# Performance work log

Measured on AMD Instinct MI355X. Metric: run time of the kernel, lower is better.

## Reference

```python
import jax, jax.numpy as jnp
import numpy as np

B, N, E = 4, 8192, 131072
R, NUM_CLASSES, H, OUT = 16, 100, 128, 32


def _rgcn_layer(h, W, src, dst, rel, mask_edge):
    # h: [B,N,in], W: [R,in,out], src/dst/rel: [B,E] int, mask_edge: [B,E]
    # Per-edge msg = h[src] @ W[rel] * norm(=1); computed as per-relation
    # projection of all nodes followed by a (src, rel) gather.
    proj = jnp.einsum('bni,rio->bnro', h, W)          # [B,N,R,out]
    bidx = jnp.arange(B)[:, None]                      # [B,1]
    msg = proj[bidx, src, rel] * mask_edge[..., None]  # [B,E,out]
    # scatter-sum messages onto destination nodes (fn.sum in DGL)
    seg = (jnp.arange(B)[:, None] * N + dst).reshape(-1)
    out = jax.ops.segment_sum(msg.reshape(B * E, -1), seg, num_segments=B * N)
    return out.reshape(B, N, -1)


def setup_inputs() -> dict:
    key = jax.random.key(0)
    ks = jax.random.split(key, 10)
    class_objects = jax.random.randint(ks[0], (B, N), 0, NUM_CLASSES)
    states_objects = jax.random.normal(ks[1], (B, N, 8), dtype=jnp.float32)
    edge_tuples = jax.random.randint(ks[2], (B, E, 2), 0, N)
    edge_classes = jax.random.randint(ks[3], (B, E), 0, R)
    mask_object = jnp.ones((B, N), dtype=jnp.float32)
    mask_edge = jnp.ones((B, E), dtype=jnp.float32)
    embed = jax.random.normal(ks[4], (NUM_CLASSES, H), dtype=jnp.float32) * 0.05
    W1 = jax.random.normal(ks[5], (R, H, H), dtype=jnp.float32) * 0.05
    W2 = jax.random.normal(ks[6], (R, H, H), dtype=jnp.float32) * 0.05
    W3 = jax.random.normal(ks[7], (R, H, OUT), dtype=jnp.float32) * 0.05
    return {'class_objects': class_objects, 'states_objects': states_objects,
            'edge_tuples': edge_tuples, 'edge_classes': edge_classes,
            'mask_object': mask_object, 'mask_edge': mask_edge,
            'embed': embed, 'W1': W1, 'W2': W2, 'W3': W3}


def reference(class_objects, states_objects, edge_tuples, edge_classes,
              mask_object, mask_edge, embed, W1, W2, W3):
    src = edge_tuples[..., 0]
    dst = edge_tuples[..., 1]
    rel = edge_classes
    h = embed[class_objects]                                  # [B,N,H]
    h = jax.nn.relu(_rgcn_layer(h, W1, src, dst, rel, mask_edge))
    h = jax.nn.relu(_rgcn_layer(h, W2, src, dst, rel, mask_edge))
    h = jax.nn.softmax(_rgcn_layer(h, W3, src, dst, rel, mask_edge), axis=-1)
    # original pads each env's node features with zeros up to max_nodes
    return h * mask_object[..., None]                         # [B,N,OUT]
```

## Files before the change

### kernel.cpp

```cpp
#include <hip/hip_runtime.h>

typedef __attribute__((ext_vector_type(4))) float f32x4;
typedef __attribute__((ext_vector_type(8))) short short8;

#define B_ 4
#define N_ 8192
#define E_ 131072
#define R_ 16
#define H_ 128
#define OUT_ 32
#define NKEYS (B_*N_*R_)
#define NEDGE (B_*E_)

__device__ __forceinline__ unsigned short f2bf(float f){
  unsigned int u = __float_as_uint(f);
  u = (u + 0x7fffu + ((u>>16)&1u)) >> 16;
  return (unsigned short)u;
}
__device__ __forceinline__ float bfh(unsigned u, int hi){
  return __uint_as_float(hi ? (u & 0xffff0000u) : (u << 16));
}
__device__ __forceinline__ unsigned cvtpk(float lo, float hi){
  unsigned r;
  asm("v_cvt_pk_bf16_f32 %0, %1, %2" : "=v"(r) : "v"(lo), "v"(hi));
  return r;
}
__device__ __forceinline__ void glds16(const void* g, void* l){
  __builtin_amdgcn_global_load_lds((const __attribute__((address_space(1))) unsigned int*)g,
                                   (__attribute__((address_space(3))) unsigned int*)l,
                                   16, 0, 0);
}


__global__ void hist_k(const int* __restrict__ et, const int* __restrict__ ec,
                       int* __restrict__ cnt){
  int e = blockIdx.x*256 + threadIdx.x;
  int b = e >> 17;
  int dst = et[2*e+1];
  int r  = ec[e];
  atomicAdd(&cnt[(((b<<13)+dst)<<4) + r], 1);
}

__global__ void scanA_k(const int* __restrict__ cnt,
                        int* __restrict__ offp, int* __restrict__ cidxp,
                        int* __restrict__ bsumV, int* __restrict__ bsumF){
  __shared__ int ldsV[256], ldsF[256];
  int t = threadIdx.x;
  int base = blockIdx.x*1024 + t*4;
  int4 v = *(const int4*)(cnt + base);
  int4 f; f.x = v.x!=0; f.y = v.y!=0; f.z = v.z!=0; f.w = v.w!=0;
  ldsV[t] = v.x+v.y+v.z+v.w;
  ldsF[t] = f.x+f.y+f.z+f.w;
  __syncthreads();
  for (int off=1; off<256; off<<=1){
    int xv = (t>=off) ? ldsV[t-off] : 0;
    int xf = (t>=off) ? ldsF[t-off] : 0;
    __syncthreads();
    ldsV[t] += xv; ldsF[t] += xf;
    __syncthreads();
  }
  if (t==255){ bsumV[blockIdx.x] = ldsV[255]; bsumF[blockIdx.x] = ldsF[255]; }
  int pv = (t==0) ? 0 : ldsV[t-1];
  int pf = (t==0) ? 0 : ldsF[t-1];
  int4 ov; ov.x = pv; ov.y = ov.x+v.x; ov.z = ov.y+v.y; ov.w = ov.z+v.z;
  int4 of; of.x = pf; of.y = of.x+f.x; of.z = of.y+f.y; of.w = of.z+f.z;
  *(int4*)(offp  + base) = ov;
  *(int4*)(cidxp + base) = of;
}

__global__ void scanB_k(int* __restrict__ bsumV, int* __restrict__ bsumF){
  int* bs = blockIdx.x ? bsumF : bsumV;
  __shared__ int lds[256];
  int t = threadIdx.x;
  int2 v = *(const int2*)(bs + t*2);
  lds[t] = v.x+v.y;
  __syncthreads();
  for (int off=1; off<256; off<<=1){
    int x = (t>=off) ? lds[t-off] : 0;
    __syncthreads();
    lds[t] += x;
    __syncthreads();
  }
  int pre = (t==0) ? 0 : lds[t-1];
  int2 o; o.x = pre; o.y = pre + v.x;
  *(int2*)(bs + t*2) = o;
}

__global__ void scanC_k(const int* __restrict__ offp, const int* __restrict__ cidxp,
                        const int* __restrict__ bsumV, const int* __restrict__ bsumF,
                        const int* __restrict__ cnt,
                        int* __restrict__ off,
                        int* __restrict__ cmapA, int* __restrict__ cmapB,
                        uint4* __restrict__ kdesc, int aggcRow){
  int t = threadIdx.x;
  int base = blockIdx.x*1024 + t*4;
  int addV = bsumV[blockIdx.x];
  int addF = bsumF[blockIdx.x] + 1;
  int4 o  = *(const int4*)(offp + base);
  o.x+=addV; o.y+=addV; o.z+=addV; o.w+=addV;
  *(int4*)(off + base) = o;
  int4 cx = *(const int4*)(cidxp + base);
  int4 cv = *(const int4*)(cnt + base);
  int4 cm;
  cm.x = cv.x ? cx.x+addF : 0;
  cm.y = cv.y ? cx.y+addF : 0;
  cm.z = cv.z ? cx.z+addF : 0;
  cm.w = cv.w ? cx.w+addF : 0;
  int4 vr;
  vr.x = aggcRow + cm.x; vr.y = aggcRow + cm.y;
  vr.z = aggcRow + cm.z; vr.w = aggcRow + cm.w;
  *(int4*)(cmapA + base) = vr;
  *(int4*)(cmapB + base) = vr;
  *(int2*)&kdesc[base+0].x = make_int2(o.x, (cv.x<<20)|cm.x);
  *(int2*)&kdesc[base+1].x = make_int2(o.y, (cv.y<<20)|cm.y);
  *(int2*)&kdesc[base+2].x = make_int2(o.z, (cv.z<<20)|cm.z);
  *(int2*)&kdesc[base+3].x = make_int2(o.w, (cv.w<<20)|cm.w);
}

__global__ void fill_k(const int* __restrict__ et, const int* __restrict__ ec,
                       const float* __restrict__ me, int* __restrict__ off,
                       uint2* __restrict__ erec, uint4* __restrict__ kdesc,
                       int* __restrict__ cmapA, int* __restrict__ cmapB,
                       int hARow, int hBRow){
  int e = blockIdx.x*256 + threadIdx.x;
  int b = e >> 17;
  int src = et[2*e];
  int dst = et[2*e+1];
  int r  = ec[e];
  int key = (((b<<13)+dst)<<4) + r;
  unsigned mbits = __float_as_uint(me[e]);
  int pos = atomicAdd(&off[key], 1);
  erec[pos] = make_uint2((unsigned)src, mbits);
  uint2 kxy = *(const uint2*)&kdesc[key].x;
  if (pos == (int)kxy.x) {
    *(uint2*)&kdesc[key].z = make_uint2((unsigned)src, mbits);
    if ((kxy.y >> 20) == 1u && mbits == 0x3f800000u) {
      int noderow = (b<<13) + src;
      cmapA[key] = hARow + noderow;
      cmapB[key] = hBRow + noderow;
    }
  }
}


__global__ void prep_k(const int* __restrict__ cls, const float* __restrict__ emb,
                       const float* __restrict__ W1, const float* __restrict__ W2,
                       const float* __restrict__ W3,
                       unsigned short* __restrict__ h,
                       unsigned short* __restrict__ W1t,
                       unsigned short* __restrict__ W2t,
                       unsigned short* __restrict__ W3t,
                       unsigned short* __restrict__ aggc){
  int t = blockIdx.x*256 + threadIdx.x;
  if (blockIdx.x == 0 && threadIdx.x < 16) {
    *(uint4*)((char*)aggc + threadIdx.x*16) = make_uint4(0,0,0,0);
  }
  if (t < B_*N_*32) {
    int node = t>>5, c = t&31;
    int cl = cls[node];
    float4 v = *(const float4*)(emb + cl*H_ + c*4);
    uint2 o;
    o.x = f2bf(v.x) | ((unsigned int)f2bf(v.y)<<16);
    o.y = f2bf(v.z) | ((unsigned int)f2bf(v.w)<<16);
    *(uint2*)(h + node*H_ + c*4) = o;
  } else {
    int u = t - B_*N_*32;
    if (u < R_*H_*H_) {
      int k = u & 127, n = (u>>7) & 127, r = u >> 14;
      W1t[u] = f2bf(W1[(r*H_ + k)*H_ + n]);
    } else if (u < 2*R_*H_*H_) {
      int u2 = u - R_*H_*H_;
      int k = u2 & 127, n = (u2>>7) & 127, r = u2 >> 14;
      W2t[u2] = f2bf(W2[(r*H_ + k)*H_ + n]);
    } else {
      int u2 = u - 2*R_*H_*H_;
      if (u2 < R_*OUT_*H_) {
        int k = u2 & 127, n = (u2>>7) & 31, r = u2 >> 12;
        W3t[u2] = f2bf(W3[(r*H_ + k)*OUT_ + n]);
      }
    }
  }
}


__global__ __launch_bounds__(256) void agg_k(
    const unsigned short* __restrict__ h_in,
    const uint4* __restrict__ kdesc,
    const uint2* __restrict__ erec,
    unsigned short* __restrict__ aggc){
  const int orig = blockIdx.x;
  const int x    = orig & 7;
  const int b    = x >> 1;
  const int lb   = ((x & 1) << 10) + (orig >> 3);
  const int key  = (b << 17) + (lb << 6) + (threadIdx.x >> 2);
  const int q    = threadIdx.x & 3;
  uint4 kd = kdesc[key];
  int cnt = (int)(kd.y >> 20);
  if (cnt == 0) return;
  if (cnt == 1 && kd.w == 0x3f800000u) return;
  int cm = (int)(kd.y & 0xFFFFFu);
  const unsigned short* hb = h_in + ((size_t)b << 20);

  float fa[32];
  #pragma unroll
  for (int i=0;i<32;++i) fa[i] = 0.f;

#define UNP8(FP, V, M) do { \
  (FP)[0]+=M*bfh((V).x,0); (FP)[1]+=M*bfh((V).x,1); \
  (FP)[2]+=M*bfh((V).y,0); (FP)[3]+=M*bfh((V).y,1); \
  (FP)[4]+=M*bfh((V).z,0); (FP)[5]+=M*bfh((V).z,1); \
  (FP)[6]+=M*bfh((V).w,0); (FP)[7]+=M*bfh((V).w,1); \
} while(0)
#define MAC32(SRC, MB) do { \
  float m_ = __uint_as_float(MB); \
  const uint4* hp_ = (const uint4*)(hb + (((unsigned)(SRC))<<7) + (q<<5)); \
  uint4 v0_ = hp_[0], v1_ = hp_[1], v2_ = hp_[2], v3_ = hp_[3]; \
  UNP8(fa+0,  v0_, m_); UNP8(fa+8,  v1_, m_); \
  UNP8(fa+16, v2_, m_); UNP8(fa+24, v3_, m_); \
} while(0)

  int s = (int)kd.x;
  uint2 rc;
  if (cnt > 1) rc = erec[s+1];
  MAC32(kd.z, kd.w);
  for (int e = 1; e < cnt; ++e) {
    uint2 cur = rc;
    if (e+1 < cnt) rc = erec[s+e+1];
    MAC32(cur.x, cur.y);
  }
#undef MAC32
#undef UNP8

  unsigned short* ap = aggc + ((size_t)cm << 7) + (q<<5);
  #pragma unroll
  for (int c = 0; c < 4; ++c) {
    uint4 pk;
    pk.x = cvtpk(fa[c*8+0], fa[c*8+1]);
    pk.y = cvtpk(fa[c*8+2], fa[c*8+3]);
    pk.z = cvtpk(fa[c*8+4], fa[c*8+5]);
    pk.w = cvtpk(fa[c*8+6], fa[c*8+7]);
    *(uint4*)(ap + c*8) = pk;
  }
}


template<int NOUT>
__global__ __launch_bounds__((NOUT==128) ? 1024 : 512, 4) void gemm_k(
    const unsigned short* __restrict__ base,
    const int* __restrict__ cmap,
    const unsigned short* __restrict__ Wt,
    const float* __restrict__ mobj,
    unsigned short* __restrict__ h_out,
    float* __restrict__ out)
{
  constexpr int MT  = (NOUT==128) ? 128 : 64;
  constexpr int MI  = (NOUT==128) ? 2 : 1;
  constexpr int NIw = (NOUT==128) ? 2 : 1;
  __shared__ __align__(16) unsigned short A_s[3][MT*64];
  __shared__ __align__(16) unsigned short B_s[3][NOUT*64];
  __shared__ int cmap_s[MT*16];
  __shared__ float comb[(NOUT==32) ? 64*33 : 1];

  const int tid  = threadIdx.x;
  const int lane = tid & 63;
  const int w    = tid >> 6;
  const int c16  = lane & 15;
  const int g    = lane >> 4;
  const int m0   = blockIdx.x * MT;
  const int mbase = (NOUT==128) ? ((w>>2)<<5) : ((w>>1)<<4);
  const int nbase = (NOUT==128) ? ((w&3)<<5) : ((w&1)<<4);

  *(int2*)&cmap_s[tid<<1] = *(const int2*)(cmap + m0*16 + (tid<<1));
  __syncthreads();

#define STAGE(KC, BUF) do { \
  const int kc_ = (KC); \
  { \
    int m_ = tid>>3, u_ = tid&7; \
    int cm_ = cmap_s[(m_<<4) + (kc_>>1)]; \
    glds16((const char*)base + ((size_t)cm_<<8) + ((kc_&1)<<7) + ((u_ ^ (m_&7))<<4), \
           &A_s[BUF][tid<<3]); \
  } \
  if constexpr (NOUT==128) { \
    int n_ = tid>>3, u_ = tid&7; \
    glds16((const char*)Wt + ((size_t)((kc_>>1)*128 + n_)<<8) + ((kc_&1)<<7) + ((u_ ^ (n_&7))<<4), \
           &B_s[BUF][tid<<3]); \
  } else { \
    if (w < 4) { \
      int uid_ = (w<<6) + lane; \
      int n_ = uid_>>3, u_ = uid_&7; \
      glds16((const char*)Wt + ((size_t)((kc_>>1)*32 + n_)<<8) + ((kc_&1)<<7) + ((u_ ^ (n_&7))<<4), \
             &B_s[BUF][uid_<<3]); } \
  } \
} while(0)

#define WAIT_MAIN do { \
  if constexpr (NOUT==128) { asm volatile("s_waitcnt vmcnt(4)" ::: "memory"); } \
  else { if (w < 4) asm volatile("s_waitcnt vmcnt(4)" ::: "memory"); \
         else       asm volatile("s_waitcnt vmcnt(2)" ::: "memory"); } \
} while(0)
#define WAIT_T1 do { \
  if constexpr (NOUT==128) { asm volatile("s_waitcnt vmcnt(2)" ::: "memory"); } \
  else { if (w < 4) asm volatile("s_waitcnt vmcnt(2)" ::: "memory"); \
         else       asm volatile("s_waitcnt vmcnt(1)" ::: "memory"); } \
} while(0)

  f32x4 acc[MI][NIw];
  #pragma unroll
  for (int mi=0; mi<MI; ++mi)
    #pragma unroll
    for (int ni=0; ni<NIw; ++ni)
      acc[mi][ni] = f32x4{0.f,0.f,0.f,0.f};

#define COMPUTE(BUF) do { \
  _Pragma("unroll") \
  for (int kk=0; kk<2; ++kk) { \
    short8 af[MI], bfr[NIw]; \
    _Pragma("unroll") \
    for (int mi=0; mi<MI; ++mi) { \
      int m_ = mbase + mi*16 + c16; \
      af[mi] = *(const short8*)((const char*)&A_s[BUF][0] + m_*128 \
               + (((kk<<6) + (g<<4)) ^ ((m_&7)<<4))); } \
    _Pragma("unroll") \
    for (int ni=0; ni<NIw; ++ni) { \
      int n_ = nbase + ni*16 + c16; \
      bfr[ni] = *(const short8*)((const char*)&B_s[BUF][0] + n_*128 \
               + (((kk<<6) + (g<<4)) ^ ((n_&7)<<4))); } \
    _Pragma("unroll") \
    for (int mi=0; mi<MI; ++mi) \
      _Pragma("unroll") \
      for (int ni=0; ni<NIw; ++ni) \
        acc[mi][ni] = __builtin_amdgcn_mfma_f32_16x16x32_bf16(af[mi], bfr[ni], acc[mi][ni], 0,0,0); \
  } \
} while(0)

  STAGE(0, 0);
  STAGE(1, 1);
  for (int kc = 0; kc < 30; ++kc) {
    STAGE(kc+2, (kc+2)%3);
    WAIT_MAIN;
    __builtin_amdgcn_s_barrier();
    COMPUTE(kc%3);
    asm volatile("s_waitcnt lgkmcnt(0)" ::: "memory");
    __builtin_amdgcn_s_barrier();
  }
  WAIT_T1;
  __builtin_amdgcn_s_barrier();
  COMPUTE(0);
  asm volatile("s_waitcnt lgkmcnt(0)" ::: "memory");
  __builtin_amdgcn_s_barrier();
  asm volatile("s_waitcnt vmcnt(0)" ::: "memory");
  __builtin_amdgcn_s_barrier();
  COMPUTE(1);

  if constexpr (NOUT == 128) {
    #pragma unroll
    for (int mi=0; mi<MI; ++mi)
      #pragma unroll
      for (int ni=0; ni<NIw; ++ni)
        #pragma unroll
        for (int j=0; j<4; ++j) {
          int row = mbase + mi*16 + (g<<2) + j;
          int col = nbase + ni*16 + c16;
          h_out[((size_t)(m0+row)<<7) + col] = f2bf(fmaxf(acc[mi][ni][j], 0.f));
        }
  } else {
    #pragma unroll
    for (int j=0; j<4; ++j)
      comb[(mbase + (g<<2) + j)*33 + nbase + c16] = acc[0][0][j];
    __syncthreads();
    if (tid < 64) {
      const int row = tid;
      float v[32];
      #pragma unroll
      for (int c=0; c<32; ++c) v[c] = comb[row*33 + c];
      float mx = v[0];
      #pragma unroll
      for (int c=1; c<32; ++c) mx = fmaxf(mx, v[c]);
      float sm = 0.f;
      #pragma unroll
      for (int c=0; c<32; ++c){ v[c] = __expf(v[c]-mx); sm += v[c]; }
      float sc = mobj[m0+row] / sm;
      float4* op = (float4*)(out + ((size_t)(m0+row)<<5));
      #pragma unroll
      for (int c=0; c<8; ++c)
        op[c] = make_float4(v[4*c]*sc, v[4*c+1]*sc, v[4*c+2]*sc, v[4*c+3]*sc);
    }
  }
#undef STAGE
#undef WAIT_MAIN
#undef WAIT_T1
#undef COMPUTE
}

extern "C" void kernel_launch(void* const* d_in, const int* in_sizes, int n_in,
                              void* d_out, int out_size, void* d_ws, size_t ws_size,
                              hipStream_t stream){
  const int*   cls   = (const int*)  d_in[0];
  const int*   et    = (const int*)  d_in[2];
  const int*   ec    = (const int*)  d_in[3];
  const float* mobj  = (const float*)d_in[4];
  const float* medge = (const float*)d_in[5];
  const float* emb   = (const float*)d_in[6];
  const float* W1    = (const float*)d_in[7];
  const float* W2    = (const float*)d_in[8];
  const float* W3    = (const float*)d_in[9];
  float* out = (float*)d_out;

  char* ws = (char*)d_ws;
  size_t o = 0;
  auto alloc = [&](size_t bytes)->char*{
    char* p = ws + o;
    o += (bytes + 255) & ~(size_t)255;
    return p;
  };
  unsigned short* hA    = (unsigned short*)alloc((size_t)B_*N_*H_*2);
  unsigned short* hB    = (unsigned short*)alloc((size_t)B_*N_*H_*2);
  unsigned short* W1t   = (unsigned short*)alloc((size_t)R_*H_*H_*2);
  unsigned short* W2t   = (unsigned short*)alloc((size_t)R_*H_*H_*2);
  unsigned short* W3t   = (unsigned short*)alloc((size_t)R_*OUT_*H_*2);
  int*            cnt   = (int*)alloc((size_t)NKEYS*4);
  int*            off   = (int*)alloc((size_t)NKEYS*4);
  int*            offp  = (int*)alloc((size_t)NKEYS*4);
  int*            cidxp = (int*)alloc((size_t)NKEYS*4);
  int*            cmapA = (int*)alloc((size_t)NKEYS*4);
  int*            cmapB = (int*)alloc((size_t)NKEYS*4);
  int*            bsumV = (int*)alloc(512*4);
  int*            bsumF = (int*)alloc(512*4);
  uint4*          kdesc = (uint4*)alloc((size_t)NKEYS*16);
  uint2*          erec  = (uint2*)alloc((size_t)NEDGE*8);
  unsigned short* aggc  = (unsigned short*)alloc(((size_t)NKEYS+1)*H_*2);
  (void)ws_size; (void)in_sizes; (void)n_in; (void)out_size;

  const int hARow   = (int)(((char*)hA   - ws) >> 8);
  const int hBRow   = (int)(((char*)hB   - ws) >> 8);
  const int aggcRow = (int)(((char*)aggc - ws) >> 8);
  const unsigned short* vbase = (const unsigned short*)ws;

  hipMemsetAsync(cnt, 0, (size_t)NKEYS*4, stream);
  hipLaunchKernelGGL(hist_k,  dim3(NEDGE/256), dim3(256), 0, stream, et, ec, cnt);
  hipLaunchKernelGGL(scanA_k, dim3(512), dim3(256), 0, stream, cnt, offp, cidxp, bsumV, bsumF);
  hipLaunchKernelGGL(scanB_k, dim3(2),   dim3(256), 0, stream, bsumV, bsumF);
  hipLaunchKernelGGL(scanC_k, dim3(512), dim3(256), 0, stream, offp, cidxp, bsumV, bsumF,
                     cnt, off, cmapA, cmapB, kdesc, aggcRow);
  hipLaunchKernelGGL(fill_k,  dim3(NEDGE/256), dim3(256), 0, stream, et, ec, medge, off,
                     erec, kdesc, cmapA, cmapB, hARow, hBRow);

  hipLaunchKernelGGL(prep_k, dim3((B_*N_*32 + 2*R_*H_*H_ + R_*OUT_*H_)/256), dim3(256), 0, stream,
                     cls, emb, W1, W2, W3, hA, W1t, W2t, W3t, aggc);

  const int aggGrid = (NKEYS*4)/256;
  const int g128    = (B_*N_)/128;
  const int g32     = (B_*N_)/64;

  hipLaunchKernelGGL(agg_k, dim3(aggGrid), dim3(256), 0, stream, hA, kdesc, erec, aggc);
  hipLaunchKernelGGL((gemm_k<128>), dim3(g128), dim3(1024), 0, stream,
                     vbase, cmapA, W1t, (const float*)nullptr, hB, (float*)nullptr);
  hipLaunchKernelGGL(agg_k, dim3(aggGrid), dim3(256), 0, stream, hB, kdesc, erec, aggc);
  hipLaunchKernelGGL((gemm_k<128>), dim3(g128), dim3(1024), 0, stream,
                     vbase, cmapB, W2t, (const float*)nullptr, hA, (float*)nullptr);
  hipLaunchKernelGGL(agg_k, dim3(aggGrid), dim3(256), 0, stream, hA, kdesc, erec, aggc);
  hipLaunchKernelGGL((gemm_k<32>), dim3(g32), dim3(512), 0, stream,
                     vbase, cmapA, W3t, mobj, (unsigned short*)nullptr, out);
}
```

Before: 237.8 us.

## Replace counting-sort CSR build with atomicExch linked lists per key

```diff
diff --git a/kernel.cpp b/kernel.cpp
--- a/kernel.cpp
+++ b/kernel.cpp
@@ -11,6 +11,7 @@
 #define OUT_ 32
 #define NKEYS (B_*N_*R_)
 #define NEDGE (B_*E_)
+#define NEXT_MASK 0x7FFFFu
 
 __device__ __forceinline__ unsigned short f2bf(float f){
   unsigned int u = __float_as_uint(f);
@@ -32,114 +33,40 @@
 }
 
 
-__global__ void hist_k(const int* __restrict__ et, const int* __restrict__ ec,
-                       int* __restrict__ cnt){
+__global__ void link_k(const int* __restrict__ et, const int* __restrict__ ec,
+                       int* __restrict__ head, unsigned* __restrict__ link){
   int e = blockIdx.x*256 + threadIdx.x;
   int b = e >> 17;
-  int dst = et[2*e+1];
+  int2 sd = *(const int2*)(et + 2*e);
   int r  = ec[e];
-  atomicAdd(&cnt[(((b<<13)+dst)<<4) + r], 1);
-}
-
-__global__ void scanA_k(const int* __restrict__ cnt,
-                        int* __restrict__ offp, int* __restrict__ cidxp,
-                        int* __restrict__ bsumV, int* __restrict__ bsumF){
-  __shared__ int ldsV[256], ldsF[256];
-  int t = threadIdx.x;
-  int base = blockIdx.x*1024 + t*4;
-  int4 v = *(const int4*)(cnt + base);
-  int4 f; f.x = v.x!=0; f.y = v.y!=0; f.z = v.z!=0; f.w = v.w!=0;
-  ldsV[t] = v.x+v.y+v.z+v.w;
-  ldsF[t] = f.x+f.y+f.z+f.w;
-  __syncthreads();
-  for (int off=1; off<256; off<<=1){
-    int xv = (t>=off) ? ldsV[t-off] : 0;
-    int xf = (t>=off) ? ldsF[t-off] : 0;
-    __syncthreads();
-    ldsV[t] += xv; ldsF[t] += xf;
-    __syncthreads();
-  }
-  if (t==255){ bsumV[blockIdx.x] = ldsV[255]; bsumF[blockIdx.x] = ldsF[255]; }
-  int pv = (t==0) ? 0 : ldsV[t-1];
-  int pf = (t==0) ? 0 : ldsF[t-1];
-  int4 ov; ov.x = pv; ov.y = ov.x+v.x; ov.z = ov.y+v.y; ov.w = ov.z+v.z;
-  int4 of; of.x = pf; of.y = of.x+f.x; of.z = of.y+f.y; of.w = of.z+f.z;
-  *(int4*)(offp  + base) = ov;
-  *(int4*)(cidxp + base) = of;
-}
-
-__global__ void scanB_k(int* __restrict__ bsumV, int* __restrict__ bsumF){
-  int* bs = blockIdx.x ? bsumF : bsumV;
-  __shared__ int lds[256];
-  int t = threadIdx.x;
-  int2 v = *(const int2*)(bs + t*2);
-  lds[t] = v.x+v.y;
-  __syncthreads();
-  for (int off=1; off<256; off<<=1){
-    int x = (t>=off) ? lds[t-off] : 0;
-    __syncthreads();
-    lds[t] += x;
-    __syncthreads();
-  }
-  int pre = (t==0) ? 0 : lds[t-1];
-  int2 o; o.x = pre; o.y = pre + v.x;
-  *(int2*)(bs + t*2) = o;
-}
-
-__global__ void scanC_k(const int* __restrict__ offp, const int* __restrict__ cidxp,
-                        const int* __restrict__ bsumV, const int* __restrict__ bsumF,
-                        const int* __restrict__ cnt,
-                        int* __restrict__ off,
-                        int* __restrict__ cmapA, int* __restrict__ cmapB,
-                        uint4* __restrict__ kdesc, int aggcRow){
-  int t = threadIdx.x;
-  int base = blockIdx.x*1024 + t*4;
-  int addV = bsumV[blockIdx.x];
-  int addF = bsumF[blockIdx.x] + 1;
-  int4 o  = *(const int4*)(offp + base);
-  o.x+=addV; o.y+=addV; o.z+=addV; o.w+=addV;
-  *(int4*)(off + base) = o;
-  int4 cx = *(const int4*)(cidxp + base);
-  int4 cv = *(const int4*)(cnt + base);
-  int4 cm;
-  cm.x = cv.x ? cx.x+addF : 0;
-  cm.y = cv.y ? cx.y+addF : 0;
-  cm.z = cv.z ? cx.z+addF : 0;
-  cm.w = cv.w ? cx.w+addF : 0;
-  int4 vr;
-  vr.x = aggcRow + cm.x; vr.y = aggcRow + cm.y;
-  vr.z = aggcRow + cm.z; vr.w = aggcRow + cm.w;
-  *(int4*)(cmapA + base) = vr;
-  *(int4*)(cmapB + base) = vr;
-  *(int2*)&kdesc[base+0].x = make_int2(o.x, (cv.x<<20)|cm.x);
-  *(int2*)&kdesc[base+1].x = make_int2(o.y, (cv.y<<20)|cm.y);
-  *(int2*)&kdesc[base+2].x = make_int2(o.z, (cv.z<<20)|cm.z);
-  *(int2*)&kdesc[base+3].x = make_int2(o.w, (cv.w<<20)|cm.w);
-}
-
-__global__ void fill_k(const int* __restrict__ et, const int* __restrict__ ec,
-                       const float* __restrict__ me, int* __restrict__ off,
-                       uint2* __restrict__ erec, uint4* __restrict__ kdesc,
+  int key = (((b<<13)+sd.y)<<4) + r;
+  int old = atomicExch(&head[key], e);
+  unsigned nxt = (old < 0) ? (unsigned)e : (unsigned)old;
+  link[e] = (((unsigned)sd.x) << 19) | nxt;
+}
+
+
+__global__ void cmap_k(const int* __restrict__ head, const unsigned* __restrict__ link,
+                       const float* __restrict__ me,
                        int* __restrict__ cmapA, int* __restrict__ cmapB,
-                       int hARow, int hBRow){
-  int e = blockIdx.x*256 + threadIdx.x;
-  int b = e >> 17;
-  int src = et[2*e];
-  int dst = et[2*e+1];
-  int r  = ec[e];
-  int key = (((b<<13)+dst)<<4) + r;
-  unsigned mbits = __float_as_uint(me[e]);
-  int pos = atomicAdd(&off[key], 1);
-  erec[pos] = make_uint2((unsigned)src, mbits);
-  uint2 kxy = *(const uint2*)&kdesc[key].x;
-  if (pos == (int)kxy.x) {
-    *(uint2*)&kdesc[key].z = make_uint2((unsigned)src, mbits);
-    if ((kxy.y >> 20) == 1u && mbits == 0x3f800000u) {
-      int noderow = (b<<13) + src;
-      cmapA[key] = hARow + noderow;
-      cmapB[key] = hBRow + noderow;
+                       int hARow, int hBRow, int aggcRow){
+  int key = blockIdx.x*256 + threadIdx.x;
+  int hd = head[key];
+  int vA = aggcRow, vB = aggcRow;
+  if (hd >= 0) {
+    unsigned lk = link[hd];
+    int nxt = (int)(lk & NEXT_MASK);
+    if (nxt == hd && me[hd] == 1.0f) {
+      int noderow = ((key >> 17) << 13) + (int)(lk >> 19);
+      vA = hARow + noderow;
+      vB = hBRow + noderow;
+    } else {
+      vA = aggcRow + 1 + key;
+      vB = vA;
     }
   }
+  cmapA[key] = vA;
+  cmapB[key] = vB;
 }
 
 
@@ -185,8 +112,9 @@
 
 __global__ __launch_bounds__(256) void agg_k(
     const unsigned short* __restrict__ h_in,
-    const uint4* __restrict__ kdesc,
-    const uint2* __restrict__ erec,
+    const int* __restrict__ head,
+    const unsigned* __restrict__ link,
+    const float* __restrict__ me,
     unsigned short* __restrict__ aggc){
   const int orig = blockIdx.x;
   const int x    = orig & 7;
@@ -194,11 +122,12 @@
   const int lb   = ((x & 1) << 10) + (orig >> 3);
   const int key  = (b << 17) + (lb << 6) + (threadIdx.x >> 2);
   const int q    = threadIdx.x & 3;
-  uint4 kd = kdesc[key];
-  int cnt = (int)(kd.y >> 20);
-  if (cnt == 0) return;
-  if (cnt == 1 && kd.w == 0x3f800000u) return;
-  int cm = (int)(kd.y & 0xFFFFFu);
+  int hd = head[key];
+  if (hd < 0) return;
+  unsigned lk = link[hd];
+  int nxt = (int)(lk & NEXT_MASK);
+  float m0 = me[hd];
+  if (nxt == hd && m0 == 1.0f) return;
   const unsigned short* hb = h_in + ((size_t)b << 20);
 
   float fa[32];
@@ -211,27 +140,29 @@
   (FP)[4]+=M*bfh((V).z,0); (FP)[5]+=M*bfh((V).z,1); \
   (FP)[6]+=M*bfh((V).w,0); (FP)[7]+=M*bfh((V).w,1); \
 } while(0)
-#define MAC32(SRC, MB) do { \
-  float m_ = __uint_as_float(MB); \
+#define MAC32(SRC, M) do { \
   const uint4* hp_ = (const uint4*)(hb + (((unsigned)(SRC))<<7) + (q<<5)); \
   uint4 v0_ = hp_[0], v1_ = hp_[1], v2_ = hp_[2], v3_ = hp_[3]; \
-  UNP8(fa+0,  v0_, m_); UNP8(fa+8,  v1_, m_); \
-  UNP8(fa+16, v2_, m_); UNP8(fa+24, v3_, m_); \
-} while(0)
-
-  int s = (int)kd.x;
-  uint2 rc;
-  if (cnt > 1) rc = erec[s+1];
-  MAC32(kd.z, kd.w);
-  for (int e = 1; e < cnt; ++e) {
-    uint2 cur = rc;
-    if (e+1 < cnt) rc = erec[s+e+1];
-    MAC32(cur.x, cur.y);
+  UNP8(fa+0,  v0_, M); UNP8(fa+8,  v1_, M); \
+  UNP8(fa+16, v2_, M); UNP8(fa+24, v3_, M); \
+} while(0)
+
+  int cur = hd;
+  unsigned clk = lk;
+  float cm = m0;
+  for (;;) {
+    int src = (int)(clk >> 19);
+    MAC32(src, cm);
+    int nx = (int)(clk & NEXT_MASK);
+    if (nx == cur) break;
+    cur = nx;
+    clk = link[cur];
+    cm  = me[cur];
   }
 #undef MAC32
 #undef UNP8
 
-  unsigned short* ap = aggc + ((size_t)cm << 7) + (q<<5);
+  unsigned short* ap = aggc + (((size_t)(1 + key)) << 7) + (q<<5);
   #pragma unroll
   for (int c = 0; c < 4; ++c) {
     uint4 pk;
@@ -419,16 +350,10 @@
   unsigned short* W1t   = (unsigned short*)alloc((size_t)R_*H_*H_*2);
   unsigned short* W2t   = (unsigned short*)alloc((size_t)R_*H_*H_*2);
   unsigned short* W3t   = (unsigned short*)alloc((size_t)R_*OUT_*H_*2);
-  int*            cnt   = (int*)alloc((size_t)NKEYS*4);
-  int*            off   = (int*)alloc((size_t)NKEYS*4);
-  int*            offp  = (int*)alloc((size_t)NKEYS*4);
-  int*            cidxp = (int*)alloc((size_t)NKEYS*4);
+  int*            head  = (int*)alloc((size_t)NKEYS*4);
+  unsigned*       link  = (unsigned*)alloc((size_t)NEDGE*4);
   int*            cmapA = (int*)alloc((size_t)NKEYS*4);
   int*            cmapB = (int*)alloc((size_t)NKEYS*4);
-  int*            bsumV = (int*)alloc(512*4);
-  int*            bsumF = (int*)alloc(512*4);
-  uint4*          kdesc = (uint4*)alloc((size_t)NKEYS*16);
-  uint2*          erec  = (uint2*)alloc((size_t)NEDGE*8);
   unsigned short* aggc  = (unsigned short*)alloc(((size_t)NKEYS+1)*H_*2);
   (void)ws_size; (void)in_sizes; (void)n_in; (void)out_size;
 
@@ -437,14 +362,10 @@
   const int aggcRow = (int)(((char*)aggc - ws) >> 8);
   const unsigned short* vbase = (const unsigned short*)ws;
 
-  hipMemsetAsync(cnt, 0, (size_t)NKEYS*4, stream);
-  hipLaunchKernelGGL(hist_k,  dim3(NEDGE/256), dim3(256), 0, stream, et, ec, cnt);
-  hipLaunchKernelGGL(scanA_k, dim3(512), dim3(256), 0, stream, cnt, offp, cidxp, bsumV, bsumF);
-  hipLaunchKernelGGL(scanB_k, dim3(2),   dim3(256), 0, stream, bsumV, bsumF);
-  hipLaunchKernelGGL(scanC_k, dim3(512), dim3(256), 0, stream, offp, cidxp, bsumV, bsumF,
-                     cnt, off, cmapA, cmapB, kdesc, aggcRow);
-  hipLaunchKernelGGL(fill_k,  dim3(NEDGE/256), dim3(256), 0, stream, et, ec, medge, off,
-                     erec, kdesc, cmapA, cmapB, hARow, hBRow);
+  hipMemsetAsync(head, 0xFF, (size_t)NKEYS*4, stream);
+  hipLaunchKernelGGL(link_k, dim3(NEDGE/256), dim3(256), 0, stream, et, ec, head, link);
+  hipLaunchKernelGGL(cmap_k, dim3(NKEYS/256), dim3(256), 0, stream, head, link, medge,
+                     cmapA, cmapB, hARow, hBRow, aggcRow);
 
   hipLaunchKernelGGL(prep_k, dim3((B_*N_*32 + 2*R_*H_*H_ + R_*OUT_*H_)/256), dim3(256), 0, stream,
                      cls, emb, W1, W2, W3, hA, W1t, W2t, W3t, aggc);
@@ -453,13 +374,13 @@
   const int g128    = (B_*N_)/128;
   const int g32     = (B_*N_)/64;
 
-  hipLaunchKernelGGL(agg_k, dim3(aggGrid), dim3(256), 0, stream, hA, kdesc, erec, aggc);
+  hipLaunchKernelGGL(agg_k, dim3(aggGrid), dim3(256), 0, stream, hA, head, link, medge, aggc);
   hipLaunchKernelGGL((gemm_k<128>), dim3(g128), dim3(1024), 0, stream,
                      vbase, cmapA, W1t, (const float*)nullptr, hB, (float*)nullptr);
-  hipLaunchKernelGGL(agg_k, dim3(aggGrid), dim3(256), 0, stream, hB, kdesc, erec, aggc);
+  hipLaunchKernelGGL(agg_k, dim3(aggGrid), dim3(256), 0, stream, hB, head, link, medge, aggc);
   hipLaunchKernelGGL((gemm_k<128>), dim3(g128), dim3(1024), 0, stream,
                      vbase, cmapB, W2t, (const float*)nullptr, hA, (float*)nullptr);
-  hipLaunchKernelGGL(agg_k, dim3(aggGrid), dim3(256), 0, stream, hA, kdesc, erec, aggc);
+  hipLaunchKernelGGL(agg_k, dim3(aggGrid), dim3(256), 0, stream, hA, head, link, medge, aggc);
   hipLaunchKernelGGL((gemm_k<32>), dim3(g32), dim3(512), 0, stream,
                      vbase, cmapA, W3t, mobj, (unsigned short*)nullptr, out);
 }
```

New measurement: 207.2 us, median of 3. 12.9% less time.
